# Kernel tuning notes

Hardware: AMD Instinct MI355X
Metric: run time of the kernel (lower is better)

## Reference

```python
import jax, jax.numpy as jnp
import numpy as np

# Fixed graph/model dims (see shape_source)
C = 16      # cardinality
SUB = 64    # representation_size // cardinality
R = 1024    # representation_size
E = 1024    # node_encoding_size
S = 1024    # processed spatial feature size
G = 256     # global (FPN) channels
NH = 64     # number of human nodes
N = 256     # total number of nodes (humans first)
P = NH * N  # number of (human, node) pairs
EPS = 1e-5


def _layernorm(x, g, b):
    mu = jnp.mean(x, axis=-1, keepdims=True)
    var = jnp.var(x, axis=-1, keepdims=True)
    return (x - mu) * jax.lax.rsqrt(var + EPS) * g + b


def _pair_head(app, spat, W1, b1, W2, b2, W3, b3):
    # app: [P_or_1, A], spat: [P, S] -> [P, R]  (sum over cardinality; NO outer relu)
    a1 = jnp.einsum('pi,cis->cps', app, W1) + b1[:, None, :]   # [C,P_or_1,SUB]
    a2 = jnp.einsum('pj,cjs->cps', spat, W2) + b2[:, None, :]  # [C,P,SUB]
    h = jax.nn.relu(a1 * a2)                                   # broadcast over P
    return jnp.einsum('cps,csr->pr', h, W3) + jnp.sum(b3, axis=0)


def reference(node_encodings, spatial_raw, global_feat,
              sp_W1, sp_b1, sp_W2, sp_b2, sp_W3, sp_b3,
              ah_W1, ah_b1, ah_W2, ah_b2, ah_W3, ah_b3,
              o2s_W1, o2s_b1, o2s_W2, o2s_b2, o2s_W3, o2s_b3,
              s2o_W1, s2o_b1, s2o_W2, s2o_b2, s2o_W3, s2o_b3,
              ahg_W1, ahg_b1, ahg_W2, ahg_b2, ahg_W3, ahg_b3,
              adj_W, adj_b, lnh_g, lnh_b, lno_g, lno_b):
    # spatial head MLP: 36 -> 128 -> 256 -> 1024 with ReLU
    sp = jax.nn.relu(spatial_raw @ sp_W1 + sp_b1)
    sp = jax.nn.relu(sp @ sp_W2 + sp_b2)
    sp = jax.nn.relu(sp @ sp_W3 + sp_b3)            # [P, S]
    sp3 = sp.reshape(NH, N, S)                      # [NH, N, S]

    x_idx = jnp.repeat(jnp.arange(NH), N)           # [P]
    y_idx = jnp.tile(jnp.arange(N), NH)             # [P]

    h_enc = node_encodings[:NH]                     # humans are permuted to the top
    o_enc = node_encodings

    for _ in range(1):  # num_iter
        app_pairs = jnp.concatenate([h_enc[x_idx], o_enc[y_idx]], axis=1)  # [P, 2E]
        weights = jax.nn.relu(_pair_head(app_pairs, sp, ah_W1, ah_b1, ah_W2, ah_b2, ah_W3, ah_b3))
        adj = (weights @ adj_W + adj_b).reshape(NH, N)

        # obj_to_sub (node_type='object'): appearance = all node encodings
        a1 = jnp.einsum('ni,cis->cns', o_enc, o2s_W1) + o2s_b1[:, None, :]          # [C,N,SUB]
        a2 = jnp.einsum('hnj,cjs->chns', sp3, o2s_W2) + o2s_b2[:, None, None, :]    # [C,NH,N,SUB]
        m = jnp.einsum('chns,csr->hnr', jax.nn.relu(a1[:, None] * a2), o2s_W3) + jnp.sum(o2s_b3, axis=0)
        msg_h = jax.nn.relu(jnp.sum(jax.nn.softmax(adj, axis=1)[..., None] * m, axis=1))  # [NH,R]
        h_enc = _layernorm(h_enc + msg_h, lnh_g, lnh_b)

        # sub_to_obj (node_type='human'): appearance = human encodings
        a1 = jnp.einsum('hi,cis->chs', h_enc, s2o_W1) + s2o_b1[:, None, :]          # [C,NH,SUB]
        a2 = jnp.einsum('hnj,cjs->cnhs', sp3, s2o_W2) + s2o_b2[:, None, None, :]    # [C,N,NH,SUB]
        m = jnp.einsum('cnhs,csr->nhr', jax.nn.relu(a1[:, None] * a2), s2o_W3) + jnp.sum(s2o_b3, axis=0)
        msg_o = jax.nn.relu(jnp.sum(jax.nn.softmax(adj.T, axis=1)[..., None] * m, axis=1))  # [N,R]
        o_enc = _layernorm(o_enc + msg_o, lno_g, lno_b)

    app_final = jnp.concatenate([h_enc[x_idx], o_enc[y_idx]], axis=1)               # [P, 2E]
    f_local = jax.nn.relu(_pair_head(app_final, sp, ah_W1, ah_b1, ah_W2, ah_b2, ah_W3, ah_b3))
    f_glob = jax.nn.relu(_pair_head(global_feat, sp, ahg_W1, ahg_b1, ahg_W2, ahg_b2, ahg_W3, ahg_b3))
    return jnp.concatenate([f_local, f_glob], axis=1)  # [P, 2R]


def setup_inputs() -> dict:
    key = jax.random.key(0)
    ks = iter(jax.random.split(key, 64))
    def rn(shape, scale=0.05):
        return jax.random.normal(next(ks), shape, dtype=jnp.float32) * scale
    inp = {
        'node_encodings': jax.random.normal(next(ks), (N, E), dtype=jnp.float32),
        'spatial_raw': jax.random.normal(next(ks), (P, 36), dtype=jnp.float32),
        'global_feat': jax.random.normal(next(ks), (1, G), dtype=jnp.float32),
        'sp_W1': rn((36, 128)), 'sp_b1': jnp.zeros(128, jnp.float32),
        'sp_W2': rn((128, 256)), 'sp_b2': jnp.zeros(256, jnp.float32),
        'sp_W3': rn((256, S)), 'sp_b3': jnp.zeros(S, jnp.float32),
        'ah_W1': rn((C, 2 * E, SUB)), 'ah_b1': jnp.zeros((C, SUB), jnp.float32),
        'ah_W2': rn((C, S, SUB)), 'ah_b2': jnp.zeros((C, SUB), jnp.float32),
        'ah_W3': rn((C, SUB, R)), 'ah_b3': jnp.zeros((C, R), jnp.float32),
        'o2s_W1': rn((C, E, SUB)), 'o2s_b1': jnp.zeros((C, SUB), jnp.float32),
        'o2s_W2': rn((C, S, SUB)), 'o2s_b2': jnp.zeros((C, SUB), jnp.float32),
        'o2s_W3': rn((C, SUB, R)), 'o2s_b3': jnp.zeros((C, R), jnp.float32),
        's2o_W1': rn((C, E, SUB)), 's2o_b1': jnp.zeros((C, SUB), jnp.float32),
        's2o_W2': rn((C, S, SUB)), 's2o_b2': jnp.zeros((C, SUB), jnp.float32),
        's2o_W3': rn((C, SUB, R)), 's2o_b3': jnp.zeros((C, R), jnp.float32),
        'ahg_W1': rn((C, G, SUB)), 'ahg_b1': jnp.zeros((C, SUB), jnp.float32),
        'ahg_W2': rn((C, S, SUB)), 'ahg_b2': jnp.zeros((C, SUB), jnp.float32),
        'ahg_W3': rn((C, SUB, R)), 'ahg_b3': jnp.zeros((C, R), jnp.float32),
        'adj_W': rn((R, 1)), 'adj_b': jnp.zeros(1, jnp.float32),
        'lnh_g': jnp.ones(E, jnp.float32), 'lnh_b': jnp.zeros(E, jnp.float32),
        'lno_g': jnp.ones(E, jnp.float32), 'lno_b': jnp.zeros(E, jnp.float32),
    }
    return inp
```

## Files before the change

### kernel.cpp

```cpp
#include <hip/hip_runtime.h>
#include <hip/hip_bf16.h>
#include <stdint.h>
#include <stddef.h>

using bf16 = __hip_bfloat16;
typedef __bf16 bf16x8 __attribute__((ext_vector_type(8)));
typedef float f32x4 __attribute__((ext_vector_type(4)));

#define P_  16384

__device__ __forceinline__ void gload16(const void* g, void* l) {
    __builtin_amdgcn_global_load_lds((const __attribute__((address_space(1))) void*)g,
                                     (__attribute__((address_space(3))) void*)l, 16, 0, 0);
}

struct GArgs {
    const bf16* A; const bf16* B; void* C;
    const float* bias;
    const float* aux1;
    int M, N, K, ldc, kchunk;
    void* dst1; void* dst2; void* dst3; void* dstH;
    const float* cb0; const float* cb1; const float* cb2; const float* cb3;
    const float* a1gv; const float* Ahp; const float* Aop; const float* b1p;
};

template<int MODE, bool RELU, bool BIAS>
__global__ __launch_bounds__(256, 4)
void gemm_bt(GArgs g)
{
    __shared__ __align__(16) bf16 As[128 * 32];
    __shared__ __align__(16) bf16 Bs[128 * 32];

    const int tid  = threadIdx.x;
    const int wave = tid >> 6;
    const int lane = tid & 63;
    const int tileM = blockIdx.x * 128;
    const int tileN = blockIdx.y * 128;
    const int wr = (wave >> 1) << 6;
    const int wc = (wave & 1) << 6;
    const int M = g.M, N = g.N, K = g.K;

    f32x4 acc[4][4] = {};

    int arow[2], brow[2], ako[2];
    #pragma unroll
    for (int j = 0; j < 2; ++j) {
        int c  = wave * 128 + j * 64 + lane;
        int r  = c >> 2;
        ako[j] = (c & 3) << 3;
        int gr = tileM + r; if (gr > M - 1) gr = M - 1;
        arow[j] = gr;
        int gn = tileN + r; if (gn > N - 1) gn = N - 1;
        brow[j] = gn;
    }
    const int m0   = wr + (lane & 15);
    const int n0   = wc + (lane & 15);
    const int koff = (lane >> 4) << 3;

    int kbeg = 0, kend = K;
    if constexpr (MODE == 2) { kbeg = blockIdx.z * g.kchunk; kend = kbeg + g.kchunk; }

    for (int k0 = kbeg; k0 < kend; k0 += 32) {
        #pragma unroll
        for (int j = 0; j < 2; ++j) {
            int c = wave * 128 + j * 64 + lane;
            gload16(g.A + (size_t)arow[j] * K + k0 + ako[j], (void*)(As + c * 8));
            gload16(g.B + (size_t)brow[j] * K + k0 + ako[j], (void*)(Bs + c * 8));
        }
        __syncthreads();
        bf16x8 af[4], bfv[4];
        #pragma unroll
        for (int i = 0; i < 4; ++i) {
            af[i]  = *(const bf16x8*)(As + (m0 + i * 16) * 32 + koff);
            bfv[i] = *(const bf16x8*)(Bs + (n0 + i * 16) * 32 + koff);
        }
        #pragma unroll
        for (int i = 0; i < 4; ++i)
            #pragma unroll
            for (int j = 0; j < 4; ++j)
                acc[i][j] = __builtin_amdgcn_mfma_f32_16x16x32_bf16(af[i], bfv[j], acc[i][j], 0, 0, 0);
        __syncthreads();
    }

    const int rbase = tileM + wr + ((lane >> 4) << 2);
    const int cbase = tileN + wc + (lane & 15);

    if constexpr (MODE == 0 || MODE == 1) {
        #pragma unroll
        for (int i = 0; i < 4; ++i)
            #pragma unroll
            for (int j = 0; j < 4; ++j)
                #pragma unroll
                for (int r = 0; r < 4; ++r) {
                    int grow = rbase + i * 16 + r;
                    if (grow >= M) continue;
                    int gcol = cbase + j * 16;
                    float v = acc[i][j][r];
                    if (BIAS) v += g.bias[gcol];
                    if (RELU) v = fmaxf(v, 0.f);
                    if (MODE == 1) ((bf16*)g.C)[(size_t)grow * g.ldc + gcol] = __float2bfloat16(v);
                    else           ((float*)g.C)[(size_t)grow * g.ldc + gcol] = v;
                }
    } else if constexpr (MODE == 2) {
        #pragma unroll
        for (int i = 0; i < 4; ++i)
            #pragma unroll
            for (int j = 0; j < 4; ++j)
                #pragma unroll
                for (int r = 0; r < 4; ++r) {
                    int grow = rbase + i * 16 + r;
                    if (grow >= M) continue;
                    atomicAdd((float*)g.C + (size_t)grow * g.ldc + cbase + j * 16, acc[i][j][r]);
                }
    } else if constexpr (MODE == 6) {
        #pragma unroll
        for (int i = 0; i < 4; ++i)
            #pragma unroll
            for (int r = 0; r < 4; ++r) {
                float s = 0.f;
                #pragma unroll
                for (int j = 0; j < 4; ++j) {
                    int gcol = cbase + j * 16;
                    s += fmaxf(acc[i][j][r] + g.bias[gcol], 0.f) * g.aux1[gcol];
                }
                s += __shfl_xor(s, 1); s += __shfl_xor(s, 2);
                s += __shfl_xor(s, 4); s += __shfl_xor(s, 8);
                if ((lane & 15) == 0)
                    atomicAdd((float*)g.C + rbase + i * 16 + r, s);
            }
    } else if constexpr (MODE == 9) {
        int grp = tileN >> 10;
        int lcb = (tileN & 1023) + wc + (lane & 15);
        #pragma unroll
        for (int i = 0; i < 4; ++i)
            #pragma unroll
            for (int j = 0; j < 4; ++j)
                #pragma unroll
                for (int r = 0; r < 4; ++r) {
                    int p    = rbase + i * 16 + r;
                    int lcol = lcb + j * 16;
                    float accv = acc[i][j][r];
                    if (grp == 0) {
                        bf16 a2b = __float2bfloat16(accv + g.cb0[lcol]);
                        ((bf16*)g.C)[(size_t)p * 1024 + lcol] = a2b;
                        float a1 = g.Ahp[((size_t)(p >> 8)) * 1024 + lcol]
                                 + g.Aop[((size_t)(p & 255)) * 2048 + lcol] + g.b1p[lcol];
                        ((bf16*)g.dstH)[(size_t)p * 1024 + lcol] =
                            __float2bfloat16(fmaxf(a1 * (float)a2b, 0.f));
                    } else if (grp == 1) {
                        ((bf16*)g.dst1)[(size_t)p * 1024 + lcol] =
                            __float2bfloat16(accv + g.cb1[lcol]);
                    } else if (grp == 2) {
                        ((bf16*)g.dst2)[(size_t)p * 1024 + lcol] =
                            __float2bfloat16(accv + g.cb2[lcol]);
                    } else {
                        float a2v = accv + g.cb3[lcol];
                        ((bf16*)g.dst3)[(size_t)p * 1024 + lcol] =
                            __float2bfloat16(fmaxf(g.a1gv[lcol] * a2v, 0.f));
                    }
                }
    }
}

static GArgs mkargs(const bf16* A, const bf16* B, void* C, const float* bias,
                    const float* aux1, int M, int N, int K, int ldc, int kchunk)
{
    GArgs g{};
    g.A = A; g.B = B; g.C = C; g.bias = bias; g.aux1 = aux1;
    g.M = M; g.N = N; g.K = K; g.ldc = ldc; g.kchunk = kchunk;
    return g;
}

__global__ void reduce_o2s(const bf16* __restrict__ a2, const float* __restrict__ a1,
                           const float* __restrict__ b1, const float* __restrict__ sh,
                           bf16* __restrict__ out)
{
    int h = blockIdx.y, cq = blockIdx.x;
    int ng = threadIdx.x >> 5, ct = threadIdx.x & 31;
    int c = cq * 256 + ct * 8;
    float b1v[8], accv[8] = {};
    #pragma unroll
    for (int j = 0; j < 8; ++j) b1v[j] = b1[c + j];
    const float* shh = sh + h * 256;
    for (int n = ng; n < 256; n += 8) {
        float w = shh[n];
        bf16x8 a2v = *(const bf16x8*)(a2 + ((size_t)(h * 256 + n) << 10) + c);
        const float* a1p = a1 + (size_t)n * 2048 + c;
        #pragma unroll
        for (int j = 0; j < 8; ++j)
            accv[j] += w * fmaxf((a1p[j] + b1v[j]) * (float)a2v[j], 0.f);
    }
    __shared__ float red[8][264];
    #pragma unroll
    for (int j = 0; j < 8; ++j) red[ng][ct * 8 + j] = accv[j];
    __syncthreads();
    for (int s = 4; s > 0; s >>= 1) {
        if (ng < s)
            #pragma unroll
            for (int j = 0; j < 8; ++j) red[ng][ct * 8 + j] += red[ng + s][ct * 8 + j];
        __syncthreads();
    }
    if (ng == 0) {
        bf16x8 o;
        #pragma unroll
        for (int j = 0; j < 8; ++j) o[j] = (__bf16)red[0][ct * 8 + j];
        *(bf16x8*)(out + (size_t)h * 1024 + c) = o;
    }
}

__global__ void reduce_s2o(const bf16* __restrict__ a2, const float* __restrict__ a1,
                           const float* __restrict__ b1, const float* __restrict__ so,
                           bf16* __restrict__ out)
{
    int n = blockIdx.y, cq = blockIdx.x;
    int hg = threadIdx.x >> 5, ct = threadIdx.x & 31;
    int c = cq * 256 + ct * 8;
    float b1v[8], accv[8] = {};
    #pragma unroll
    for (int j = 0; j < 8; ++j) b1v[j] = b1[c + j];
    const float* son = so + n * 64;
    #pragma unroll
    for (int hh = 0; hh < 8; ++hh) {
        int h = hg + hh * 8;
        float w = son[h];
        bf16x8 a2v = *(const bf16x8*)(a2 + ((size_t)(h * 256 + n) << 10) + c);
        const float* a1p = a1 + (size_t)h * 2048 + c;
        #pragma unroll
        for (int j = 0; j < 8; ++j)
            accv[j] += w * fmaxf((a1p[j] + b1v[j]) * (float)a2v[j], 0.f);
    }
    __shared__ float red[8][264];
    #pragma unroll
    for (int j = 0; j < 8; ++j) red[hg][ct * 8 + j] = accv[j];
    __syncthreads();
    for (int s = 4; s > 0; s >>= 1) {
        if (hg < s)
            #pragma unroll
            for (int j = 0; j < 8; ++j) red[hg][ct * 8 + j] += red[hg + s][ct * 8 + j];
        __syncthreads();
    }
    if (hg == 0) {
        bf16x8 o;
        #pragma unroll
        for (int j = 0; j < 8; ++j) o[j] = (__bf16)red[0][ct * 8 + j];
        *(bf16x8*)(out + (size_t)n * 1024 + c) = o;
    }
}

__global__ void transp(const float* __restrict__ src, bf16* __restrict__ dst,
                       int rows, int cols, size_t sstride, size_t dstride)
{
    const float* s = src + blockIdx.z * sstride;
    bf16*        d = dst + blockIdx.z * dstride;
    __shared__ float tile[32][33];
    int c0 = blockIdx.x * 32, r0 = blockIdx.y * 32;
    int x = threadIdx.x, y = threadIdx.y;
    for (int yy = y; yy < 32; yy += 8) {
        int r = r0 + yy, c = c0 + x;
        tile[yy][x] = (r < rows && c < cols) ? s[(size_t)r * cols + c] : 0.f;
    }
    __syncthreads();
    for (int yy = y; yy < 32; yy += 8) {
        int c = c0 + yy, r = r0 + x;
        if (c < cols && r < rows) d[(size_t)c * rows + r] = __float2bfloat16(tile[x][yy]);
    }
}

struct T8 { const float* s[8]; bf16* d[8]; size_t ss[8]; };
__global__ void transp64b(T8 t)
{
    int pair = blockIdx.z >> 4, slice = blockIdx.z & 15;
    const float* s = t.s[pair] + slice * t.ss[pair];
    bf16*        d = t.d[pair] + slice * 65536;
    __shared__ float tile[32][33];
    int c0 = blockIdx.x * 32, r0 = blockIdx.y * 32;
    int x = threadIdx.x, y = threadIdx.y;
    for (int yy = y; yy < 32; yy += 8)
        tile[yy][x] = s[(size_t)(r0 + yy) * 64 + c0 + x];
    __syncthreads();
    for (int yy = y; yy < 32; yy += 8)
        d[(size_t)(c0 + yy) * 1024 + r0 + x] = __float2bfloat16(tile[x][yy]);
}

struct T4 { const float* s[4]; bf16* d[4]; };
__global__ void transp1024b(T4 t)
{
    const float* s = t.s[blockIdx.z];
    bf16*        d = t.d[blockIdx.z];
    __shared__ float tile[32][33];
    int c0 = blockIdx.x * 32, r0 = blockIdx.y * 32;
    int x = threadIdx.x, y = threadIdx.y;
    for (int yy = y; yy < 32; yy += 8)
        tile[yy][x] = s[(size_t)(r0 + yy) * 1024 + c0 + x];
    __syncthreads();
    for (int yy = y; yy < 32; yy += 8)
        d[(size_t)(c0 + yy) * 1024 + r0 + x] = __float2bfloat16(tile[x][yy]);
}

__global__ void conv_spw1(const float* __restrict__ src, bf16* __restrict__ dst) {
    int i = blockIdx.x * 256 + threadIdx.x;
    if (i >= 128 * 64) return;
    int k = i & 63, n = i >> 6;
    dst[i] = __float2bfloat16(k < 36 ? src[k * 128 + n] : 0.f);
}

__global__ void pad_spatial(const float* __restrict__ src, bf16* __restrict__ dst) {
    int i = blockIdx.x * 256 + threadIdx.x;
    int k = i & 63, p = i >> 6;
    dst[i] = __float2bfloat16(k < 36 ? src[p * 36 + k] : 0.f);
}

__global__ void cast_f2b(const float* __restrict__ src, bf16* __restrict__ dst, int n) {
    int i = blockIdx.x * 256 + threadIdx.x;
    if (i < n) dst[i] = __float2bfloat16(src[i]);
}

struct S4 { const float* s[4]; float* d[4]; };
__global__ void sumb3b(S4 a) {
    int i = blockIdx.x * 256 + threadIdx.x;
    int pair = i >> 10, r = i & 1023;
    const float* b3 = a.s[pair];
    float s = 0.f;
    #pragma unroll
    for (int c = 0; c < 16; ++c) s += b3[c * 1024 + r];
    a.d[pair][r] = s;
}

__global__ void hbuild(const float* __restrict__ Ah, int ah_ld,
                       const float* __restrict__ Ao, int ao_ld,
                       const float* __restrict__ b1, const bf16* __restrict__ a2,
                       bf16* __restrict__ H)
{
    size_t base = ((size_t)blockIdx.x * 256 + threadIdx.x) * 8;
    int cs = (int)(base & 1023);
    int p  = (int)(base >> 10);
    const float* ph = Ah + (size_t)(p >> 8) * ah_ld + cs;
    const float* po = Ao + (size_t)(p & 255) * ao_ld + cs;
    bf16x8 av = *(const bf16x8*)(a2 + base);
    bf16x8 o;
    #pragma unroll
    for (int j = 0; j < 8; ++j) {
        float a1 = ph[j] + po[j] + b1[cs + j];
        o[j] = (__bf16)fmaxf(a1 * (float)av[j], 0.f);
    }
    *(bf16x8*)(H + base) = o;
}

__global__ void softmax_h(const float* __restrict__ adj, float* __restrict__ sh) {
    int h = blockIdx.x, n = threadIdx.x;
    __shared__ float red[256];
    float v = adj[h * 256 + n];
    red[n] = v; __syncthreads();
    for (int s = 128; s > 0; s >>= 1) { if (n < s) red[n] = fmaxf(red[n], red[n + s]); __syncthreads(); }
    float m = red[0]; __syncthreads();
    float e = expf(v - m);
    red[n] = e; __syncthreads();
    for (int s = 128; s > 0; s >>= 1) { if (n < s) red[n] += red[n + s]; __syncthreads(); }
    sh[h * 256 + n] = e / red[0];
}

__global__ void softmax_o(const float* __restrict__ adj, float* __restrict__ so) {
    int n = blockIdx.x, h = threadIdx.x;
    float v = adj[h * 256 + n];
    float m = v;
    #pragma unroll
    for (int off = 32; off; off >>= 1) m = fmaxf(m, __shfl_xor(m, off));
    float e = expf(v - m);
    float s = e;
    #pragma unroll
    for (int off = 32; off; off >>= 1) s += __shfl_xor(s, off);
    so[n * 64 + h] = e / s;
}

__global__ void ln_k(const float* __restrict__ x, const float* __restrict__ msgraw,
                     const float* __restrict__ sb3,
                     const float* __restrict__ g, const float* __restrict__ bb,
                     bf16* __restrict__ out)
{
    int row = blockIdx.x, t = threadIdx.x;
    const float* xr = x + (size_t)row * 1024;
    const float* mr = msgraw + (size_t)row * 1024;
    float v[4]; float s = 0.f, ss = 0.f;
    #pragma unroll
    for (int j = 0; j < 4; ++j) {
        int i = t + j * 256;
        v[j] = xr[i] + fmaxf(mr[i] + sb3[i], 0.f);
        s += v[j]; ss += v[j] * v[j];
    }
    __shared__ float r1[256], r2[256];
    r1[t] = s; r2[t] = ss; __syncthreads();
    for (int k = 128; k > 0; k >>= 1) { if (t < k) { r1[t] += r1[t + k]; r2[t] += r2[t + k]; } __syncthreads(); }
    float mean = r1[0] * (1.f / 1024.f);
    float var  = r2[0] * (1.f / 1024.f) - mean * mean;
    float inv  = rsqrtf(var + 1e-5f);
    #pragma unroll
    for (int j = 0; j < 4; ++j) {
        int i = t + j * 256;
        out[(size_t)row * 1024 + i] = __float2bfloat16((v[j] - mean) * inv * g[i] + bb[i]);
    }
}

__global__ void a1g_k(const float* __restrict__ gf, const float* __restrict__ W1,
                      const float* __restrict__ b1, float* __restrict__ a1g)
{
    int cs = blockIdx.x * 256 + threadIdx.x;
    int c = cs >> 6, s = cs & 63;
    float acc = b1[cs];
    for (int g = 0; g < 256; ++g) acc += gf[g] * W1[((size_t)c * 256 + g) * 64 + s];
    a1g[cs] = acc;
}

extern "C" void kernel_launch(void* const* d_in, const int* in_sizes, int n_in,
                              void* d_out, int out_size, void* d_ws, size_t ws_size,
                              hipStream_t stream)
{
    const float* node_enc = (const float*)d_in[0];
    const float* spatial  = (const float*)d_in[1];
    const float* gfeat    = (const float*)d_in[2];
    const float* sp_W1 = (const float*)d_in[3];  const float* sp_b1 = (const float*)d_in[4];
    const float* sp_W2 = (const float*)d_in[5];  const float* sp_b2 = (const float*)d_in[6];
    const float* sp_W3 = (const float*)d_in[7];  const float* sp_b3 = (const float*)d_in[8];
    const float* ah_W1 = (const float*)d_in[9];  const float* ah_b1 = (const float*)d_in[10];
    const float* ah_W2 = (const float*)d_in[11]; const float* ah_b2 = (const float*)d_in[12];
    const float* ah_W3 = (const float*)d_in[13]; const float* ah_b3 = (const float*)d_in[14];
    const float* o2s_W1 = (const float*)d_in[15]; const float* o2s_b1 = (const float*)d_in[16];
    const float* o2s_W2 = (const float*)d_in[17]; const float* o2s_b2 = (const float*)d_in[18];
    const float* o2s_W3 = (const float*)d_in[19]; const float* o2s_b3 = (const float*)d_in[20];
    const float* s2o_W1 = (const float*)d_in[21]; const float* s2o_b1 = (const float*)d_in[22];
    const float* s2o_W2 = (const float*)d_in[23]; const float* s2o_b2 = (const float*)d_in[24];
    const float* s2o_W3 = (const float*)d_in[25]; const float* s2o_b3 = (const float*)d_in[26];
    const float* ahg_W1 = (const float*)d_in[27]; const float* ahg_b1 = (const float*)d_in[28];
    const float* ahg_W2 = (const float*)d_in[29]; const float* ahg_b2 = (const float*)d_in[30];
    const float* ahg_W3 = (const float*)d_in[31]; const float* ahg_b3 = (const float*)d_in[32];
    const float* adj_W = (const float*)d_in[33];
    const float* lnh_g = (const float*)d_in[35]; const float* lnh_b = (const float*)d_in[36];
    const float* lno_g = (const float*)d_in[37]; const float* lno_b = (const float*)d_in[38];

    char* w = (char*)d_ws;
    auto alloc = [&](size_t bytes) { char* p = w; w += (bytes + 255) & ~(size_t)255; return p; };
    bf16*  sp      = (bf16*)alloc((size_t)P_ * 1024 * 2);
    bf16*  a2_ah   = (bf16*)alloc((size_t)P_ * 1024 * 2);
    bf16*  Hbuf    = (bf16*)alloc((size_t)P_ * 1024 * 2);
    bf16*  a2_o2s  = (bf16*)alloc((size_t)P_ * 1024 * 2);
    bf16*  a2_s2o  = (bf16*)alloc((size_t)P_ * 1024 * 2);
    bf16*  H_ahg   = (bf16*)alloc((size_t)P_ * 1024 * 2);
    bf16*  spat_pad= (bf16*)alloc((size_t)P_ * 64 * 2);
    bf16*  spL1    = (bf16*)alloc((size_t)P_ * 128 * 2);
    bf16*  spL2    = (bf16*)alloc((size_t)P_ * 256 * 2);
    bf16*  enc_bf  = (bf16*)alloc(256 * 1024 * 2);
    bf16*  henc_bf = (bf16*)alloc(64 * 1024 * 2);
    bf16*  oenc_bf = (bf16*)alloc(256 * 1024 * 2);
    bf16*  HredH   = (bf16*)alloc(64 * 1024 * 2);
    bf16*  HredO   = (bf16*)alloc(256 * 1024 * 2);
    bf16*  spW1t   = (bf16*)alloc(128 * 64 * 2);
    bf16*  spW2t   = (bf16*)alloc(256 * 128 * 2);
    bf16*  spW3t   = (bf16*)alloc(1024 * 256 * 2);
    bf16*  W2cat   = (bf16*)alloc((size_t)4096 * 1024 * 2);
    bf16*  W1catB  = (bf16*)alloc((size_t)2048 * 1024 * 2);
    bf16*  W1catF  = (bf16*)alloc((size_t)2048 * 1024 * 2);
    bf16*  ahW3t   = (bf16*)alloc(1024 * 1024 * 2);
    bf16*  o2sW3t  = (bf16*)alloc(1024 * 1024 * 2);
    bf16*  s2oW3t  = (bf16*)alloc(1024 * 1024 * 2);
    bf16*  ahgW3t  = (bf16*)alloc(1024 * 1024 * 2);
    float* Ah    = (float*)alloc(64 * 1024 * 4);
    float* Aoa1  = (float*)alloc(256 * 2048 * 4);
    float* A1f   = (float*)alloc(64 * 2048 * 4);
    float* Ao_f  = (float*)alloc(256 * 1024 * 4);
    size_t z1_bytes = (size_t)(64 * 1024 + 256 * 2048 + 64 * 2048 + 256 * 1024) * 4 + 1024;
    float* adjv  = (float*)alloc(P_ * 4);
    float* msgh  = (float*)alloc(64 * 1024 * 4);
    float* msgo  = (float*)alloc(256 * 1024 * 4);
    size_t z2_bytes = (size_t)(P_ + 64 * 1024 + 256 * 1024) * 4 + 1024;
    float* sh    = (float*)alloc(P_ * 4);
    float* so    = (float*)alloc(P_ * 4);
    float* a1g   = (float*)alloc(1024 * 4);
    float* sb3_ah  = (float*)alloc(4096);
    float* sb3_o2s = (float*)alloc(4096);
    float* sb3_s2o = (float*)alloc(4096);
    float* sb3_ahg = (float*)alloc(4096);

    hipMemsetAsync(Ah,   0, z1_bytes, stream);
    hipMemsetAsync(adjv, 0, z2_bytes, stream);

    {
        T8 t;
        t.s[0] = ah_W1;                     t.d[0] = W1catF + (size_t)1024 * 1024; t.ss[0] = (size_t)2048 * 64;
        t.s[1] = ah_W1 + (size_t)1024 * 64; t.d[1] = W1catB;                       t.ss[1] = (size_t)2048 * 64;
        t.s[2] = o2s_W1;                    t.d[2] = W1catB + (size_t)1024 * 1024; t.ss[2] = 65536;
        t.s[3] = s2o_W1;                    t.d[3] = W1catF;                       t.ss[3] = 65536;
        t.s[4] = ah_W2;                     t.d[4] = W2cat;                        t.ss[4] = 65536;
        t.s[5] = o2s_W2;                    t.d[5] = W2cat + (size_t)1024 * 1024;  t.ss[5] = 65536;
        t.s[6] = s2o_W2;                    t.d[6] = W2cat + (size_t)2048 * 1024;  t.ss[6] = 65536;
        t.s[7] = ahg_W2;                    t.d[7] = W2cat + (size_t)3072 * 1024;  t.ss[7] = 65536;
        transp64b<<<dim3(2, 32, 128), dim3(32, 8), 0, stream>>>(t);
    }
    {
        T4 t;
        t.s[0] = ah_W3;  t.d[0] = ahW3t;
        t.s[1] = o2s_W3; t.d[1] = o2sW3t;
        t.s[2] = s2o_W3; t.d[2] = s2oW3t;
        t.s[3] = ahg_W3; t.d[3] = ahgW3t;
        transp1024b<<<dim3(32, 32, 4), dim3(32, 8), 0, stream>>>(t);
    }
    dim3 tb(32, 8);
    conv_spw1<<<32, 256, 0, stream>>>(sp_W1, spW1t);
    transp<<<dim3(8, 4, 1),  tb, 0, stream>>>(sp_W2, spW2t, 128, 256, 0, 0);
    transp<<<dim3(32, 8, 1), tb, 0, stream>>>(sp_W3, spW3t, 256, 1024, 0, 0);
    pad_spatial<<<4096, 256, 0, stream>>>(spatial, spat_pad);
    cast_f2b<<<1024, 256, 0, stream>>>(node_enc, enc_bf, 256 * 1024);
    {
        S4 a;
        a.s[0] = ah_b3;  a.d[0] = sb3_ah;
        a.s[1] = o2s_b3; a.d[1] = sb3_o2s;
        a.s[2] = s2o_b3; a.d[2] = sb3_s2o;
        a.s[3] = ahg_b3; a.d[3] = sb3_ahg;
        sumb3b<<<16, 256, 0, stream>>>(a);
    }
    a1g_k<<<4, 256, 0, stream>>>(gfeat, ahg_W1, ahg_b1, a1g);

    gemm_bt<2, false, false><<<dim3(2, 16, 16), 256, 0, stream>>>(
        mkargs(enc_bf, W1catB, Aoa1, nullptr, nullptr, 256, 2048, 1024, 2048, 64));
    gemm_bt<2, false, false><<<dim3(1, 8, 16), 256, 0, stream>>>(
        mkargs(enc_bf, W1catF + (size_t)1024 * 1024, Ah, nullptr, nullptr, 64, 1024, 1024, 1024, 64));

    gemm_bt<1, true, true><<<dim3(128, 1), 256, 0, stream>>>(
        mkargs(spat_pad, spW1t, spL1, sp_b1, nullptr, P_, 128, 64, 128, 0));
    gemm_bt<1, true, true><<<dim3(128, 2), 256, 0, stream>>>(
        mkargs(spL1, spW2t, spL2, sp_b2, nullptr, P_, 256, 128, 256, 0));
    gemm_bt<1, true, true><<<dim3(128, 8), 256, 0, stream>>>(
        mkargs(spL2, spW3t, sp, sp_b3, nullptr, P_, 1024, 256, 1024, 0));

    {
        GArgs g = mkargs(sp, W2cat, a2_ah, nullptr, nullptr, P_, 4096, 1024, 1024, 0);
        g.dst1 = a2_o2s; g.dst2 = a2_s2o; g.dst3 = H_ahg; g.dstH = Hbuf;
        g.cb0 = ah_b2; g.cb1 = o2s_b2; g.cb2 = s2o_b2; g.cb3 = ahg_b2;
        g.a1gv = a1g; g.Ahp = Ah; g.Aop = Aoa1; g.b1p = ah_b1;
        gemm_bt<9, false, false><<<dim3(128, 32), 256, 0, stream>>>(g);
    }

    gemm_bt<6, false, false><<<dim3(128, 8), 256, 0, stream>>>(
        mkargs(Hbuf, ahW3t, adjv, sb3_ah, adj_W, P_, 1024, 1024, 1024, 0));
    softmax_h<<<64, 256, 0, stream>>>(adjv, sh);
    softmax_o<<<256, 64, 0, stream>>>(adjv, so);

    reduce_o2s<<<dim3(4, 64), 256, 0, stream>>>(a2_o2s, Aoa1 + 1024, o2s_b1, sh, HredH);
    gemm_bt<2, false, false><<<dim3(1, 8, 16), 256, 0, stream>>>(
        mkargs(HredH, o2sW3t, msgh, nullptr, nullptr, 64, 1024, 1024, 1024, 64));
    ln_k<<<64, 256, 0, stream>>>(node_enc, msgh, sb3_o2s, lnh_g, lnh_b, henc_bf);

    gemm_bt<2, false, false><<<dim3(1, 16, 16), 256, 0, stream>>>(
        mkargs(henc_bf, W1catF, A1f, nullptr, nullptr, 64, 2048, 1024, 2048, 64));

    reduce_s2o<<<dim3(4, 256), 256, 0, stream>>>(a2_s2o, A1f, s2o_b1, so, HredO);
    gemm_bt<2, false, false><<<dim3(2, 8, 16), 256, 0, stream>>>(
        mkargs(HredO, s2oW3t, msgo, nullptr, nullptr, 256, 1024, 1024, 1024, 64));
    ln_k<<<256, 256, 0, stream>>>(node_enc, msgo, sb3_s2o, lno_g, lno_b, oenc_bf);

    gemm_bt<2, false, false><<<dim3(2, 8, 16), 256, 0, stream>>>(
        mkargs(oenc_bf, W1catB, Ao_f, nullptr, nullptr, 256, 1024, 1024, 1024, 64));
    hbuild<<<8192, 256, 0, stream>>>(A1f + 1024, 2048, Ao_f, 1024, ah_b1, a2_ah, Hbuf);
    gemm_bt<0, true, true><<<dim3(128, 8), 256, 0, stream>>>(
        mkargs(Hbuf, ahW3t, (float*)d_out, sb3_ah, nullptr, P_, 1024, 1024, 2048, 0));

    gemm_bt<0, true, true><<<dim3(128, 8), 256, 0, stream>>>(
        mkargs(H_ahg, ahgW3t, (float*)d_out + 1024, sb3_ahg, nullptr, P_, 1024, 1024, 2048, 0));

    (void)in_sizes; (void)n_in; (void)out_size; (void)ws_size;
}
```

Measured before the change: 802.8 us.

## Use BK=64 swizzled LDS tiles, merge first-layer GEMMs and final output GEMMs

The shared GEMM kernel now loads 64-wide K tiles with an XOR-swizzled LDS layout and runs two MFMA k-steps per barrier pair, which halves the barrier count and is meant to reduce LDS bank conflicts. The two initial node-encoding projections are merged into one GEMM over a three-part concatenated weight, and the two final output GEMMs are combined into one launch using blockIdx.z to pick operands. The split-K chunk is now hardcoded to 64 in mode 2. LDS use per block doubles, which may lower occupancy.

New measurement: 795.8 us. About the same (-0.9%).

```diff
diff --git a/kernel.cpp b/kernel.cpp
--- a/kernel.cpp
+++ b/kernel.cpp
@@ -28,8 +28,8 @@
 __global__ __launch_bounds__(256, 4)
 void gemm_bt(GArgs g)
 {
-    __shared__ __align__(16) bf16 As[128 * 32];
-    __shared__ __align__(16) bf16 Bs[128 * 32];
+    __shared__ __align__(16) bf16 As[128 * 64];
+    __shared__ __align__(16) bf16 Bs[128 * 64];
 
     const int tid  = threadIdx.x;
     const int wave = tid >> 6;
@@ -40,45 +40,53 @@
     const int wc = (wave & 1) << 6;
     const int M = g.M, N = g.N, K = g.K;
 
+    const bf16* Ap = g.A; const bf16* Bp = g.B;
+    void* Cp = g.C; const float* biasp = g.bias;
+    if (MODE == 0 && blockIdx.z == 1) {
+        Ap = (const bf16*)g.dst1; Bp = (const bf16*)g.dst2;
+        Cp = g.dst3; biasp = g.cb1;
+    }
+
     f32x4 acc[4][4] = {};
 
-    int arow[2], brow[2], ako[2];
-    #pragma unroll
-    for (int j = 0; j < 2; ++j) {
-        int c  = wave * 128 + j * 64 + lane;
-        int r  = c >> 2;
-        ako[j] = (c & 3) << 3;
-        int gr = tileM + r; if (gr > M - 1) gr = M - 1;
-        arow[j] = gr;
-        int gn = tileN + r; if (gn > N - 1) gn = N - 1;
-        brow[j] = gn;
-    }
-    const int m0   = wr + (lane & 15);
-    const int n0   = wc + (lane & 15);
-    const int koff = (lane >> 4) << 3;
+    const int gk = (((lane & 7) ^ (lane >> 3)) << 3);
+    int arow[4], brow[4];
+    #pragma unroll
+    for (int j = 0; j < 4; ++j) {
+        int r = wave * 32 + j * 8 + (lane >> 3);
+        int gr = tileM + r; if (gr > M - 1) gr = M - 1; arow[j] = gr;
+        int gn = tileN + r; if (gn > N - 1) gn = N - 1; brow[j] = gn;
+    }
+    const int m0 = wr + (lane & 15);
+    const int n0 = wc + (lane & 15);
+    const int q  = lane >> 4;
 
     int kbeg = 0, kend = K;
-    if constexpr (MODE == 2) { kbeg = blockIdx.z * g.kchunk; kend = kbeg + g.kchunk; }
-
-    for (int k0 = kbeg; k0 < kend; k0 += 32) {
-        #pragma unroll
-        for (int j = 0; j < 2; ++j) {
-            int c = wave * 128 + j * 64 + lane;
-            gload16(g.A + (size_t)arow[j] * K + k0 + ako[j], (void*)(As + c * 8));
-            gload16(g.B + (size_t)brow[j] * K + k0 + ako[j], (void*)(Bs + c * 8));
+    if constexpr (MODE == 2) { kbeg = blockIdx.z * 64; kend = kbeg + 64; }
+
+    for (int k0 = kbeg; k0 < kend; k0 += 64) {
+        #pragma unroll
+        for (int j = 0; j < 4; ++j) {
+            int c = wave * 256 + j * 64 + lane;
+            gload16(Ap + (size_t)arow[j] * K + k0 + gk, (void*)(As + c * 8));
+            gload16(Bp + (size_t)brow[j] * K + k0 + gk, (void*)(Bs + c * 8));
         }
         __syncthreads();
-        bf16x8 af[4], bfv[4];
-        #pragma unroll
-        for (int i = 0; i < 4; ++i) {
-            af[i]  = *(const bf16x8*)(As + (m0 + i * 16) * 32 + koff);
-            bfv[i] = *(const bf16x8*)(Bs + (n0 + i * 16) * 32 + koff);
+        #pragma unroll
+        for (int kk = 0; kk < 2; ++kk) {
+            const int gs = ((kk << 2) + q) ^ (lane & 7);
+            bf16x8 af[4], bfv[4];
+            #pragma unroll
+            for (int i = 0; i < 4; ++i) {
+                af[i]  = *(const bf16x8*)(As + (m0 + i * 16) * 64 + gs * 8);
+                bfv[i] = *(const bf16x8*)(Bs + (n0 + i * 16) * 64 + gs * 8);
+            }
+            #pragma unroll
+            for (int i = 0; i < 4; ++i)
+                #pragma unroll
+                for (int j = 0; j < 4; ++j)
+                    acc[i][j] = __builtin_amdgcn_mfma_f32_16x16x32_bf16(af[i], bfv[j], acc[i][j], 0, 0, 0);
         }
-        #pragma unroll
-        for (int i = 0; i < 4; ++i)
-            #pragma unroll
-            for (int j = 0; j < 4; ++j)
-                acc[i][j] = __builtin_amdgcn_mfma_f32_16x16x32_bf16(af[i], bfv[j], acc[i][j], 0, 0, 0);
         __syncthreads();
     }
 
@@ -96,10 +104,10 @@
                     if (grow >= M) continue;
                     int gcol = cbase + j * 16;
                     float v = acc[i][j][r];
-                    if (BIAS) v += g.bias[gcol];
+                    if (BIAS) v += biasp[gcol];
                     if (RELU) v = fmaxf(v, 0.f);
-                    if (MODE == 1) ((bf16*)g.C)[(size_t)grow * g.ldc + gcol] = __float2bfloat16(v);
-                    else           ((float*)g.C)[(size_t)grow * g.ldc + gcol] = v;
+                    if (MODE == 1) ((bf16*)Cp)[(size_t)grow * g.ldc + gcol] = __float2bfloat16(v);
+                    else           ((float*)Cp)[(size_t)grow * g.ldc + gcol] = v;
                 }
     } else if constexpr (MODE == 2) {
         #pragma unroll
@@ -110,7 +118,7 @@
                 for (int r = 0; r < 4; ++r) {
                     int grow = rbase + i * 16 + r;
                     if (grow >= M) continue;
-                    atomicAdd((float*)g.C + (size_t)grow * g.ldc + cbase + j * 16, acc[i][j][r]);
+                    atomicAdd((float*)Cp + (size_t)grow * g.ldc + cbase + j * 16, acc[i][j][r]);
                 }
     } else if constexpr (MODE == 6) {
         #pragma unroll
@@ -121,12 +129,12 @@
                 #pragma unroll
                 for (int j = 0; j < 4; ++j) {
                     int gcol = cbase + j * 16;
-                    s += fmaxf(acc[i][j][r] + g.bias[gcol], 0.f) * g.aux1[gcol];
+                    s += fmaxf(acc[i][j][r] + biasp[gcol], 0.f) * g.aux1[gcol];
                 }
                 s += __shfl_xor(s, 1); s += __shfl_xor(s, 2);
                 s += __shfl_xor(s, 4); s += __shfl_xor(s, 8);
                 if ((lane & 15) == 0)
-                    atomicAdd((float*)g.C + rbase + i * 16 + r, s);
+                    atomicAdd((float*)Cp + rbase + i * 16 + r, s);
             }
     } else if constexpr (MODE == 9) {
         int grp = tileN >> 10;
@@ -142,9 +150,9 @@
                     float accv = acc[i][j][r];
                     if (grp == 0) {
                         bf16 a2b = __float2bfloat16(accv + g.cb0[lcol]);
-                        ((bf16*)g.C)[(size_t)p * 1024 + lcol] = a2b;
-                        float a1 = g.Ahp[((size_t)(p >> 8)) * 1024 + lcol]
-                                 + g.Aop[((size_t)(p & 255)) * 2048 + lcol] + g.b1p[lcol];
+                        ((bf16*)Cp)[(size_t)p * 1024 + lcol] = a2b;
+                        float a1 = g.Ahp[((size_t)(p >> 8)) * 3072 + lcol]
+                                 + g.Aop[((size_t)(p & 255)) * 3072 + lcol] + g.b1p[lcol];
                         ((bf16*)g.dstH)[(size_t)p * 1024 + lcol] =
                             __float2bfloat16(fmaxf(a1 * (float)a2b, 0.f));
                     } else if (grp == 1) {
@@ -185,7 +193,7 @@
     for (int n = ng; n < 256; n += 8) {
         float w = shh[n];
         bf16x8 a2v = *(const bf16x8*)(a2 + ((size_t)(h * 256 + n) << 10) + c);
-        const float* a1p = a1 + (size_t)n * 2048 + c;
+        const float* a1p = a1 + (size_t)n * 3072 + c;
         #pragma unroll
         for (int j = 0; j < 8; ++j)
             accv[j] += w * fmaxf((a1p[j] + b1v[j]) * (float)a2v[j], 0.f);
@@ -266,8 +274,8 @@
     }
 }
 
-struct T8 { const float* s[8]; bf16* d[8]; size_t ss[8]; };
-__global__ void transp64b(T8 t)
+struct T9 { const float* s[9]; bf16* d[9]; size_t ss[9]; };
+__global__ void transp64b(T9 t)
 {
     int pair = blockIdx.z >> 4, slice = blockIdx.z & 15;
     const float* s = t.s[pair] + slice * t.ss[pair];
@@ -456,17 +464,16 @@
     bf16*  spW2t   = (bf16*)alloc(256 * 128 * 2);
     bf16*  spW3t   = (bf16*)alloc(1024 * 256 * 2);
     bf16*  W2cat   = (bf16*)alloc((size_t)4096 * 1024 * 2);
-    bf16*  W1catB  = (bf16*)alloc((size_t)2048 * 1024 * 2);
+    bf16*  W1cat3  = (bf16*)alloc((size_t)3072 * 1024 * 2);
     bf16*  W1catF  = (bf16*)alloc((size_t)2048 * 1024 * 2);
     bf16*  ahW3t   = (bf16*)alloc(1024 * 1024 * 2);
     bf16*  o2sW3t  = (bf16*)alloc(1024 * 1024 * 2);
     bf16*  s2oW3t  = (bf16*)alloc(1024 * 1024 * 2);
     bf16*  ahgW3t  = (bf16*)alloc(1024 * 1024 * 2);
-    float* Ah    = (float*)alloc(64 * 1024 * 4);
-    float* Aoa1  = (float*)alloc(256 * 2048 * 4);
+    float* Aoa1x = (float*)alloc(256 * 3072 * 4);
     float* A1f   = (float*)alloc(64 * 2048 * 4);
     float* Ao_f  = (float*)alloc(256 * 1024 * 4);
-    size_t z1_bytes = (size_t)(64 * 1024 + 256 * 2048 + 64 * 2048 + 256 * 1024) * 4 + 1024;
+    size_t z1_bytes = (size_t)(256 * 3072 + 64 * 2048 + 256 * 1024) * 4 + 1024;
     float* adjv  = (float*)alloc(P_ * 4);
     float* msgh  = (float*)alloc(64 * 1024 * 4);
     float* msgo  = (float*)alloc(256 * 1024 * 4);
@@ -479,20 +486,21 @@
     float* sb3_s2o = (float*)alloc(4096);
     float* sb3_ahg = (float*)alloc(4096);
 
-    hipMemsetAsync(Ah,   0, z1_bytes, stream);
-    hipMemsetAsync(adjv, 0, z2_bytes, stream);
+    hipMemsetAsync(Aoa1x, 0, z1_bytes, stream);
+    hipMemsetAsync(adjv,  0, z2_bytes, stream);
 
     {
-        T8 t;
-        t.s[0] = ah_W1;                     t.d[0] = W1catF + (size_t)1024 * 1024; t.ss[0] = (size_t)2048 * 64;
-        t.s[1] = ah_W1 + (size_t)1024 * 64; t.d[1] = W1catB;                       t.ss[1] = (size_t)2048 * 64;
-        t.s[2] = o2s_W1;                    t.d[2] = W1catB + (size_t)1024 * 1024; t.ss[2] = 65536;
+        T9 t;
+        t.s[0] = ah_W1;                     t.d[0] = W1cat3 + (size_t)2048 * 1024; t.ss[0] = (size_t)2048 * 64;
+        t.s[1] = ah_W1 + (size_t)1024 * 64; t.d[1] = W1cat3;                       t.ss[1] = (size_t)2048 * 64;
+        t.s[2] = o2s_W1;                    t.d[2] = W1cat3 + (size_t)1024 * 1024; t.ss[2] = 65536;
         t.s[3] = s2o_W1;                    t.d[3] = W1catF;                       t.ss[3] = 65536;
-        t.s[4] = ah_W2;                     t.d[4] = W2cat;                        t.ss[4] = 65536;
-        t.s[5] = o2s_W2;                    t.d[5] = W2cat + (size_t)1024 * 1024;  t.ss[5] = 65536;
-        t.s[6] = s2o_W2;                    t.d[6] = W2cat + (size_t)2048 * 1024;  t.ss[6] = 65536;
-        t.s[7] = ahg_W2;                    t.d[7] = W2cat + (size_t)3072 * 1024;  t.ss[7] = 65536;
-        transp64b<<<dim3(2, 32, 128), dim3(32, 8), 0, stream>>>(t);
+        t.s[4] = ah_W1;                     t.d[4] = W1catF + (size_t)1024 * 1024; t.ss[4] = (size_t)2048 * 64;
+        t.s[5] = ah_W2;                     t.d[5] = W2cat;                        t.ss[5] = 65536;
+        t.s[6] = o2s_W2;                    t.d[6] = W2cat + (size_t)1024 * 1024;  t.ss[6] = 65536;
+        t.s[7] = s2o_W2;                    t.d[7] = W2cat + (size_t)2048 * 1024;  t.ss[7] = 65536;
+        t.s[8] = ahg_W2;                    t.d[8] = W2cat + (size_t)3072 * 1024;  t.ss[8] = 65536;
+        transp64b<<<dim3(2, 32, 144), dim3(32, 8), 0, stream>>>(t);
     }
     {
         T4 t;
@@ -518,10 +526,8 @@
     }
     a1g_k<<<4, 256, 0, stream>>>(gfeat, ahg_W1, ahg_b1, a1g);
 
-    gemm_bt<2, false, false><<<dim3(2, 16, 16), 256, 0, stream>>>(
-        mkargs(enc_bf, W1catB, Aoa1, nullptr, nullptr, 256, 2048, 1024, 2048, 64));
-    gemm_bt<2, false, false><<<dim3(1, 8, 16), 256, 0, stream>>>(
-        mkargs(enc_bf, W1catF + (size_t)1024 * 1024, Ah, nullptr, nullptr, 64, 1024, 1024, 1024, 64));
+    gemm_bt<2, false, false><<<dim3(2, 24, 16), 256, 0, stream>>>(
+        mkargs(enc_bf, W1cat3, Aoa1x, nullptr, nullptr, 256, 3072, 1024, 3072, 64));
 
     gemm_bt<1, true, true><<<dim3(128, 1), 256, 0, stream>>>(
         mkargs(spat_pad, spW1t, spL1, sp_b1, nullptr, P_, 128, 64, 128, 0));
@@ -534,7 +540,7 @@
         GArgs g = mkargs(sp, W2cat, a2_ah, nullptr, nullptr, P_, 4096, 1024, 1024, 0);
         g.dst1 = a2_o2s; g.dst2 = a2_s2o; g.dst3 = H_ahg; g.dstH = Hbuf;
         g.cb0 = ah_b2; g.cb1 = o2s_b2; g.cb2 = s2o_b2; g.cb3 = ahg_b2;
-        g.a1gv = a1g; g.Ahp = Ah; g.Aop = Aoa1; g.b1p = ah_b1;
+        g.a1gv = a1g; g.Ahp = Aoa1x + 2048; g.Aop = Aoa1x; g.b1p = ah_b1;
         gemm_bt<9, false, false><<<dim3(128, 32), 256, 0, stream>>>(g);
     }
 
@@ -543,7 +549,7 @@
     softmax_h<<<64, 256, 0, stream>>>(adjv, sh);
     softmax_o<<<256, 64, 0, stream>>>(adjv, so);
 
-    reduce_o2s<<<dim3(4, 64), 256, 0, stream>>>(a2_o2s, Aoa1 + 1024, o2s_b1, sh, HredH);
+    reduce_o2s<<<dim3(4, 64), 256, 0, stream>>>(a2_o2s, Aoa1x + 1024, o2s_b1, sh, HredH);
     gemm_bt<2, false, false><<<dim3(1, 8, 16), 256, 0, stream>>>(
         mkargs(HredH, o2sW3t, msgh, nullptr, nullptr, 64, 1024, 1024, 1024, 64));
     ln_k<<<64, 256, 0, stream>>>(node_enc, msgh, sb3_o2s, lnh_g, lnh_b, henc_bf);
@@ -557,13 +563,15 @@
     ln_k<<<256, 256, 0, stream>>>(node_enc, msgo, sb3_s2o, lno_g, lno_b, oenc_bf);
 
     gemm_bt<2, false, false><<<dim3(2, 8, 16), 256, 0, stream>>>(
-        mkargs(oenc_bf, W1catB, Ao_f, nullptr, nullptr, 256, 1024, 1024, 1024, 64));
+        mkargs(oenc_bf, W1cat3, Ao_f, nullptr, nullptr, 256, 1024, 1024, 1024, 64));
     hbuild<<<8192, 256, 0, stream>>>(A1f + 1024, 2048, Ao_f, 1024, ah_b1, a2_ah, Hbuf);
-    gemm_bt<0, true, true><<<dim3(128, 8), 256, 0, stream>>>(
-        mkargs(Hbuf, ahW3t, (float*)d_out, sb3_ah, nullptr, P_, 1024, 1024, 2048, 0));
-
-    gemm_bt<0, true, true><<<dim3(128, 8), 256, 0, stream>>>(
-        mkargs(H_ahg, ahgW3t, (float*)d_out + 1024, sb3_ahg, nullptr, P_, 1024, 1024, 2048, 0));
+
+    {
+        GArgs g = mkargs(Hbuf, ahW3t, (float*)d_out, sb3_ah, nullptr, P_, 1024, 1024, 2048, 0);
+        g.dst1 = (void*)H_ahg; g.dst2 = (void*)ahgW3t;
+        g.dst3 = (void*)((float*)d_out + 1024); g.cb1 = sb3_ahg;
+        gemm_bt<0, true, true><<<dim3(128, 8, 2), 256, 0, stream>>>(g);
+    }
 
     (void)in_sizes; (void)n_in; (void)out_size; (void)ws_size;
 }
```
